# Kernel tuning notes

Hardware: AMD Instinct MI355X
Metric: run time of the kernel (lower is better)

Reference implementation:

```python
import jax, jax.numpy as jnp
import numpy as np


def setup_inputs() -> dict:
    key = jax.random.key(0)
    k1, k2, k3 = jax.random.split(key, 3)
    N, C, H, W, K = 64, 128, 64, 64, 64
    x = jax.random.normal(k1, (N, C, H, W), dtype=jnp.float32)
    conv_w = jax.random.normal(k2, (K, C), dtype=jnp.float32) * 0.05
    centroids = jax.random.uniform(k3, (K, C), dtype=jnp.float32)
    return {"x": x, "conv_w": conv_w, "centroids": centroids}


def reference(x, conv_w, centroids):
    # x: [N, C, H, W]; conv_w: [K, C] (1x1 conv, no bias); centroids: [K, C]
    n, c = x.shape[:2]
    x_flat = x.reshape(n, c, -1)                      # [N, C, S]
    # 1x1 conv == per-pixel linear map, then softmax over clusters
    logits = jnp.einsum('kc,ncs->nks', conv_w, x_flat)  # [N, K, S]
    a = jax.nn.softmax(logits, axis=1)                  # softmax over K
    # VLAD: sum_s a[n,k,s] * (x[n,:,s] - centroid[k])
    #     = (a @ x^T) - (sum_s a) * centroid   -- two batched GEMMs, no [N,K,C,S] blowup
    vlad = jnp.einsum('nks,ncs->nkc', a, x_flat) - a.sum(axis=-1)[..., None] * centroids[None]
    # intra-normalization (L2 per cluster), flatten, global L2
    vlad = vlad / jnp.linalg.norm(vlad, axis=2, keepdims=True)
    vlad = vlad.reshape(n, -1)
    vlad = vlad / jnp.linalg.norm(vlad, axis=1, keepdims=True)
    return vlad
```

## Files before the change

### kernel.cpp

```cpp
#include <hip/hip_runtime.h>


#define Nn 64
#define Cc 128
#define Ss 4096
#define Kk 64
#define TS 64
#define CH 8
#define SB (TS*CH)
#define Pp 8

typedef __attribute__((ext_vector_type(8))) short bf16x8;
typedef __attribute__((ext_vector_type(4))) float f32x4;

__device__ __forceinline__ unsigned cvt2(float a, float b) {
  unsigned r;
  asm("v_cvt_pk_bf16_f32 %0, %1, %2" : "=v"(r) : "v"(a), "v"(b));
  return r;
}

__device__ __forceinline__ void bar_lds() {
  asm volatile("s_waitcnt lgkmcnt(0)\n\ts_barrier" ::: "memory");
}

#define XCS_STR 72
#define AKS_STR 72

__launch_bounds__(256, 2)
__global__ void netvlad_main(const float* __restrict__ x,
                             const float* __restrict__ w,
                             float* __restrict__ vlad,
                             float* __restrict__ asum,
                             int use_atomic)
{
  __shared__ __align__(16) unsigned short x_cs[2][Cc][XCS_STR];
  __shared__ __align__(16) unsigned short a_ks[Kk][AKS_STR];

  const int t   = threadIdx.x;
  const int wv  = t >> 6;
  const int l15 = t & 15;
  const int l4  = (t >> 4) & 3;
  const int n   = blockIdx.y;
  const int sb  = blockIdx.x;
  const size_t xbase = (size_t)n * Cc * Ss;

  bf16x8 wfrag[4][4];
#pragma unroll
  for (int mt = 0; mt < 4; ++mt) {
#pragma unroll
    for (int q = 0; q < 4; ++q) {
      const float* wp = w + (16*mt + l15) * Cc + 32*q + 8*l4;
      float4 a = *(const float4*)wp;
      float4 b = *(const float4*)(wp + 4);
      int4 pk = make_int4((int)cvt2(a.x, a.y), (int)cvt2(a.z, a.w),
                          (int)cvt2(b.x, b.y), (int)cvt2(b.z, b.w));
      wfrag[mt][q] = *(bf16x8*)&pk;
    }
  }

  f32x4 acc3[4][2];
#pragma unroll
  for (int mt = 0; mt < 4; ++mt)
#pragma unroll
    for (int tc = 0; tc < 2; ++tc) acc3[mt][tc] = (f32x4){0.f,0.f,0.f,0.f};
  float asum_reg[4][4];
#pragma unroll
  for (int mt = 0; mt < 4; ++mt)
#pragma unroll
    for (int r = 0; r < 4; ++r) asum_reg[mt][r] = 0.f;

  const int s4 = 4 * l15;
  const int cb = t >> 4;
  const float* px0 = x + xbase + (size_t)cb * Ss + sb * SB + s4;
  float4 v[8];
#pragma unroll
  for (int it = 0; it < 8; ++it)
    v[it] = *(const float4*)(px0 + (size_t)(16 * it) * Ss);

  for (int ch = 0; ch < CH; ++ch) {
    const int buf = ch & 1;

#pragma unroll
    for (int it = 0; it < 8; ++it) {
      float4 vv = v[it];
      unsigned p0 = cvt2(vv.x, vv.y);
      unsigned p1 = cvt2(vv.z, vv.w);
      *(int2*)&x_cs[buf][cb + 16*it][s4] = make_int2((int)p0, (int)p1);
    }
    if (ch + 1 < CH) {
      const float* px = px0 + (ch + 1) * TS;
#pragma unroll
      for (int it = 0; it < 8; ++it)
        v[it] = *(const float4*)(px + (size_t)(16 * it) * Ss);
    }
    bar_lds();

    bf16x8 bfr[4];
#pragma unroll
    for (int j = 0; j < 4; ++j) {
      const int c8 = 32*j + 8*l4;
      unsigned short h[8];
#pragma unroll
      for (int i = 0; i < 8; ++i) {
        const int i2 = (i + 2*l4) & 7;
        h[i2] = x_cs[buf][c8 + i2][16*wv + l15];
      }
      bf16x8 f;
#pragma unroll
      for (int i = 0; i < 8; ++i) f[i] = (short)h[i];
      bfr[j] = f;
    }

    f32x4 acc1[4];
#pragma unroll
    for (int mt = 0; mt < 4; ++mt) acc1[mt] = (f32x4){0.f,0.f,0.f,0.f};
#pragma unroll
    for (int q = 0; q < 4; ++q) {
#pragma unroll
      for (int mt = 0; mt < 4; ++mt)
        acc1[mt] = __builtin_amdgcn_mfma_f32_16x16x32_bf16(wfrag[mt][q], bfr[q], acc1[mt], 0, 0, 0);
    }

    float e[4][4];
    float cs = 0.f;
#pragma unroll
    for (int mt = 0; mt < 4; ++mt)
#pragma unroll
      for (int r = 0; r < 4; ++r) {
        float ev = __expf(acc1[mt][r]);
        e[mt][r] = ev;
        cs += ev;
      }
    cs += __shfl_xor(cs, 16, 64);
    cs += __shfl_xor(cs, 32, 64);
    const float inv = 1.0f / cs;
#pragma unroll
    for (int mt = 0; mt < 4; ++mt)
#pragma unroll
      for (int r = 0; r < 4; ++r) {
        float an = e[mt][r] * inv;
        asum_reg[mt][r] += an;
        a_ks[16*mt + 4*l4 + r][16*wv + l15] = (unsigned short)cvt2(an, an);
      }
    bar_lds();

#pragma unroll
    for (int q2 = 0; q2 < 2; ++q2) {
      bf16x8 afr[4];
#pragma unroll
      for (int mt = 0; mt < 4; ++mt)
        afr[mt] = *(bf16x8*)&a_ks[16*mt + l15][32*q2 + 8*l4];
#pragma unroll
      for (int tc = 0; tc < 2; ++tc) {
        bf16x8 bfx = *(bf16x8*)&x_cs[buf][32*wv + 16*tc + l15][32*q2 + 8*l4];
#pragma unroll
        for (int mt = 0; mt < 4; ++mt)
          acc3[mt][tc] = __builtin_amdgcn_mfma_f32_16x16x32_bf16(afr[mt], bfx, acc3[mt][tc], 0, 0, 0);
      }
    }
  }

  bar_lds();
  float* asml = (float*)a_ks;
#pragma unroll
  for (int mt = 0; mt < 4; ++mt) {
#pragma unroll
    for (int r = 0; r < 4; ++r) {
      float vv = asum_reg[mt][r];
      vv += __shfl_xor(vv, 1, 64);
      vv += __shfl_xor(vv, 2, 64);
      vv += __shfl_xor(vv, 4, 64);
      vv += __shfl_xor(vv, 8, 64);
      if (l15 == 0) asml[wv * Kk + 16*mt + 4*l4 + r] = vv;
    }
  }
  bar_lds();
  if (t < Kk) {
    float s = asml[t] + asml[Kk + t] + asml[2*Kk + t] + asml[3*Kk + t];
    if (use_atomic) atomicAdd(&asum[n * Kk + t], s);
    else            asum[((size_t)sb * Nn + n) * Kk + t] = s;
  }

  if (use_atomic) {
#pragma unroll
    for (int mt = 0; mt < 4; ++mt)
#pragma unroll
      for (int tc = 0; tc < 2; ++tc)
#pragma unroll
        for (int r = 0; r < 4; ++r) {
          const int k = 16*mt + 4*l4 + r;
          const int c = 32*wv + 16*tc + l15;
          atomicAdd(&vlad[((size_t)n * Kk + k) * Cc + c], acc3[mt][tc][r]);
        }
  } else {
    float* vp = vlad + ((size_t)sb * Nn + n) * (Kk * Cc);
#pragma unroll
    for (int mt = 0; mt < 4; ++mt)
#pragma unroll
      for (int tc = 0; tc < 2; ++tc)
#pragma unroll
        for (int r = 0; r < 4; ++r) {
          const int k = 16*mt + 4*l4 + r;
          const int c = 32*wv + 16*tc + l15;
          vp[k * Cc + c] = acc3[mt][tc][r];
        }
  }
}

__global__ void netvlad_epilogue(const float* __restrict__ vlad,
                                 const float* __restrict__ asum,
                                 const float* __restrict__ cent,
                                 float* __restrict__ out,
                                 int nparts)
{
  const int n  = blockIdx.x;
  const int k  = 16*blockIdx.y + (threadIdx.x >> 4);
  const int cq = threadIdx.x & 15;

  float ak = 0.f;
  float4 x0 = make_float4(0.f, 0.f, 0.f, 0.f);
  float4 x1 = make_float4(0.f, 0.f, 0.f, 0.f);
  for (int p = 0; p < nparts; ++p) {
    ak += asum[((size_t)p * Nn + n) * Kk + k];
    const float* vp = vlad + (((size_t)p * Nn + n) * Kk + k) * Cc + 8*cq;
    float4 a0 = *(const float4*)vp;
    float4 a1 = *(const float4*)(vp + 4);
    x0.x += a0.x; x0.y += a0.y; x0.z += a0.z; x0.w += a0.w;
    x1.x += a1.x; x1.y += a1.y; x1.z += a1.z; x1.w += a1.w;
  }

  const size_t cbse = (size_t)k * Cc + 8*cq;
  float4 c0 = *(const float4*)(cent + cbse);
  float4 c1 = *(const float4*)(cent + cbse + 4);
  float4 r0, r1;
  r0.x = x0.x - ak*c0.x; r0.y = x0.y - ak*c0.y; r0.z = x0.z - ak*c0.z; r0.w = x0.w - ak*c0.w;
  r1.x = x1.x - ak*c1.x; r1.y = x1.y - ak*c1.y; r1.z = x1.z - ak*c1.z; r1.w = x1.w - ak*c1.w;
  float ss = r0.x*r0.x + r0.y*r0.y + r0.z*r0.z + r0.w*r0.w
           + r1.x*r1.x + r1.y*r1.y + r1.z*r1.z + r1.w*r1.w;
  ss += __shfl_xor(ss, 1, 64);
  ss += __shfl_xor(ss, 2, 64);
  ss += __shfl_xor(ss, 4, 64);
  ss += __shfl_xor(ss, 8, 64);
  const float rn = rsqrtf(ss) * 0.125f;
  r0.x *= rn; r0.y *= rn; r0.z *= rn; r0.w *= rn;
  r1.x *= rn; r1.y *= rn; r1.z *= rn; r1.w *= rn;
  float* op = out + (size_t)n * (Kk * Cc) + (size_t)k * Cc + 8*cq;
  *(float4*)op = r0;
  *(float4*)(op + 4) = r1;
}

extern "C" void kernel_launch(void* const* d_in, const int* in_sizes, int n_in,
                              void* d_out, int out_size, void* d_ws, size_t ws_size,
                              hipStream_t stream)
{
  const float* x    = (const float*)d_in[0];
  const float* w    = (const float*)d_in[1];
  const float* cent = (const float*)d_in[2];
  float* out = (float*)d_out;

  const size_t vlad_elems_p = (size_t)Pp * Nn * Kk * Cc;
  const size_t asum_elems_p = (size_t)Pp * Nn * Kk;
  const size_t need = (vlad_elems_p + asum_elems_p) * sizeof(float);

  if (ws_size >= need) {
    float* vlad_part = (float*)d_ws;
    float* asum_part = vlad_part + vlad_elems_p;
    netvlad_main<<<dim3(Pp, Nn), 256, 0, stream>>>(x, w, vlad_part, asum_part, 0);
    netvlad_epilogue<<<dim3(Nn, 4), 256, 0, stream>>>(vlad_part, asum_part, cent, out, Pp);
  } else {
    float* vlad = (float*)d_ws;
    float* asum = vlad + (size_t)Nn * Kk * Cc;
    const size_t zbytes = ((size_t)Nn * Kk * Cc + (size_t)Nn * Kk) * sizeof(float);
    hipMemsetAsync(d_ws, 0, zbytes, stream);
    netvlad_main<<<dim3(Pp, Nn), 256, 0, stream>>>(x, w, vlad, asum, 1);
    netvlad_epilogue<<<dim3(Nn, 4), 256, 0, stream>>>(vlad, asum, cent, out, 1);
  }
}
```

Measured before the change: 207.4 us.

## Stage x tiles into LDS as fp32 via async global_load_lds

```diff
diff --git a/kernel.cpp b/kernel.cpp
--- a/kernel.cpp
+++ b/kernel.cpp
@@ -19,11 +19,20 @@
   return r;
 }
 
+__device__ __forceinline__ void gload_lds4(const float* g, float* l) {
+  __builtin_amdgcn_global_load_lds(
+      (const __attribute__((address_space(1))) void*)g,
+      (__attribute__((address_space(3))) void*)l, 4, 0, 0);
+}
+
 __device__ __forceinline__ void bar_lds() {
   asm volatile("s_waitcnt lgkmcnt(0)\n\ts_barrier" ::: "memory");
 }
-
-#define XCS_STR 72
+__device__ __forceinline__ void bar_full() {
+  asm volatile("s_waitcnt vmcnt(0) lgkmcnt(0)\n\ts_barrier" ::: "memory");
+}
+
+#define XF_STR 68
 #define AKS_STR 72
 
 __launch_bounds__(256, 2)
@@ -33,16 +42,19 @@
                              float* __restrict__ asum,
                              int use_atomic)
 {
-  __shared__ __align__(16) unsigned short x_cs[2][Cc][XCS_STR];
+  __shared__ __align__(16) float xf32[2][Cc][XF_STR];
   __shared__ __align__(16) unsigned short a_ks[Kk][AKS_STR];
 
-  const int t   = threadIdx.x;
-  const int wv  = t >> 6;
-  const int l15 = t & 15;
-  const int l4  = (t >> 4) & 3;
-  const int n   = blockIdx.y;
-  const int sb  = blockIdx.x;
+  const int t    = threadIdx.x;
+  const int wv   = t >> 6;
+  const int lane = t & 63;
+  const int l15  = t & 15;
+  const int l4   = (t >> 4) & 3;
+  const int n    = blockIdx.y;
+  const int sb   = blockIdx.x;
   const size_t xbase = (size_t)n * Cc * Ss;
+
+  const float* gx = x + xbase + (size_t)sb * SB + lane;
 
   bf16x8 wfrag[4][4];
 #pragma unroll
@@ -69,46 +81,40 @@
 #pragma unroll
     for (int r = 0; r < 4; ++r) asum_reg[mt][r] = 0.f;
 
-  const int s4 = 4 * l15;
-  const int cb = t >> 4;
-  const float* px0 = x + xbase + (size_t)cb * Ss + sb * SB + s4;
-  float4 v[8];
-#pragma unroll
-  for (int it = 0; it < 8; ++it)
-    v[it] = *(const float4*)(px0 + (size_t)(16 * it) * Ss);
+  auto stage = [&](int buf, int ch) {
+#pragma unroll
+    for (int i = 0; i < 32; ++i) {
+      const int c = 32*wv + i;
+      gload_lds4(gx + (size_t)c * Ss + ch * TS, &xf32[buf][c][0]);
+    }
+  };
+
+  stage(0, 0);
 
   for (int ch = 0; ch < CH; ++ch) {
     const int buf = ch & 1;
 
-#pragma unroll
-    for (int it = 0; it < 8; ++it) {
-      float4 vv = v[it];
-      unsigned p0 = cvt2(vv.x, vv.y);
-      unsigned p1 = cvt2(vv.z, vv.w);
-      *(int2*)&x_cs[buf][cb + 16*it][s4] = make_int2((int)p0, (int)p1);
-    }
-    if (ch + 1 < CH) {
-      const float* px = px0 + (ch + 1) * TS;
-#pragma unroll
-      for (int it = 0; it < 8; ++it)
-        v[it] = *(const float4*)(px + (size_t)(16 * it) * Ss);
-    }
-    bar_lds();
-
+    bar_full();
+
+    if (ch + 1 < CH) stage(buf ^ 1, ch + 1);
+
+    const int scol = 16*wv + l15;
     bf16x8 bfr[4];
 #pragma unroll
     for (int j = 0; j < 4; ++j) {
       const int c8 = 32*j + 8*l4;
-      unsigned short h[8];
+      float h[8];
 #pragma unroll
       for (int i = 0; i < 8; ++i) {
         const int i2 = (i + 2*l4) & 7;
-        h[i2] = x_cs[buf][c8 + i2][16*wv + l15];
-      }
-      bf16x8 f;
-#pragma unroll
-      for (int i = 0; i < 8; ++i) f[i] = (short)h[i];
-      bfr[j] = f;
+        h[i2] = xf32[buf][c8 + i2][scol];
+      }
+      int4 pk;
+      pk.x = (int)cvt2(h[0], h[1]);
+      pk.y = (int)cvt2(h[2], h[3]);
+      pk.z = (int)cvt2(h[4], h[5]);
+      pk.w = (int)cvt2(h[6], h[7]);
+      bfr[j] = *(bf16x8*)&pk;
     }
 
     f32x4 acc1[4];
@@ -152,7 +158,12 @@
         afr[mt] = *(bf16x8*)&a_ks[16*mt + l15][32*q2 + 8*l4];
 #pragma unroll
       for (int tc = 0; tc < 2; ++tc) {
-        bf16x8 bfx = *(bf16x8*)&x_cs[buf][32*wv + 16*tc + l15][32*q2 + 8*l4];
+        const float* xr = &xf32[buf][32*wv + 16*tc + l15][32*q2 + 8*l4];
+        float4 xa = *(const float4*)xr;
+        float4 xb = *(const float4*)(xr + 4);
+        int4 pk = make_int4((int)cvt2(xa.x, xa.y), (int)cvt2(xa.z, xa.w),
+                            (int)cvt2(xb.x, xb.y), (int)cvt2(xb.z, xb.w));
+        bf16x8 bfx = *(bf16x8*)&pk;
 #pragma unroll
         for (int mt = 0; mt < 4; ++mt)
           acc3[mt][tc] = __builtin_amdgcn_mfma_f32_16x16x32_bf16(afr[mt], bfx, acc3[mt][tc], 0, 0, 0);
```

Measured after the change: 212.6 us. +2.5%, slower.
